# Optimization experiments

Hardware: AMD Instinct MI355X
Metric: run time of the kernel (lower is better)

## Reference

```python
import jax, jax.numpy as jnp
import numpy as np

K = 256
TAU = 1.0


def setup_inputs() -> dict:
    key = jax.random.key(0)
    scores = jax.random.normal(key, (32, 2048), dtype=jnp.float32)
    return {"scores": scores}


def reference(scores) -> jnp.ndarray:
    # scores: [B, dim]
    bsize, dim = scores.shape
    s = scores[:, :, None]  # [B, dim, 1]
    # B_i = sum_j |s_i - s_j|  -> [B, dim, 1]
    A = jnp.abs(s - scores[:, None, :])  # [B, dim, dim]
    Bsum = jnp.sum(A, axis=-1, keepdims=True)  # [B, dim, 1]
    # scaling: (dim + 1 - 2*(i+1)) for i in 0..k-1
    scaling = (dim + 1 - 2 * (jnp.arange(K) + 1)).astype(scores.dtype)  # [k]
    C = s * scaling[None, None, :]  # [B, dim, k] (outer product)
    P_max = jnp.transpose(C - Bsum, (0, 2, 1))  # [B, k, dim]
    P_hat = jax.nn.softmax(P_max / TAU, axis=-1)
    return P_hat
```

## Files before the change

### kernel.cpp

```cpp
#include <hip/hip_runtime.h>
#include <math.h>

#define DIM 2048
#define NB 32
#define NK 256

typedef float vf4 __attribute__((ext_vector_type(4)));

__global__ __launch_bounds__(256) void bsum_kernel(const float* __restrict__ scores,
                                                   float* __restrict__ bsum) {
    __shared__ vf4 srow[128];
    const int b  = blockIdx.z;
    const int j0 = blockIdx.y * 512;
    const int i0 = blockIdx.x * 1024;
    const float* __restrict__ row = scores + b * DIM;

    if (threadIdx.x < 128) srow[threadIdx.x] = ((const vf4*)(row + j0))[threadIdx.x];
    __syncthreads();

    const vf4 xi = ((const vf4*)(row + i0))[threadIdx.x];
    float a0 = 0.f, a1 = 0.f, a2 = 0.f, a3 = 0.f;
    #pragma unroll 4
    for (int jj = 0; jj < 128; ++jj) {
        const vf4 xj = srow[jj];
        a0 += (fabsf(xi.x - xj.x) + fabsf(xi.x - xj.y)) + (fabsf(xi.x - xj.z) + fabsf(xi.x - xj.w));
        a1 += (fabsf(xi.y - xj.x) + fabsf(xi.y - xj.y)) + (fabsf(xi.y - xj.z) + fabsf(xi.y - xj.w));
        a2 += (fabsf(xi.z - xj.x) + fabsf(xi.z - xj.y)) + (fabsf(xi.z - xj.z) + fabsf(xi.z - xj.w));
        a3 += (fabsf(xi.w - xj.x) + fabsf(xi.w - xj.y)) + (fabsf(xi.w - xj.z) + fabsf(xi.w - xj.w));
    }
    float* dst = bsum + b * DIM + i0 + threadIdx.x * 4;
    atomicAdd(dst + 0, a0);
    atomicAdd(dst + 1, a1);
    atomicAdd(dst + 2, a2);
    atomicAdd(dst + 3, a3);
}

__global__ __launch_bounds__(256) void softmax_kernel(const float* __restrict__ scores,
                                                      const float* __restrict__ bsum,
                                                      float* __restrict__ out) {
    const int b = blockIdx.y;
    const int w = threadIdx.x >> 6;
    const int t = threadIdx.x & 63;
    const int k = blockIdx.x * 4 + w;
    const float scale = (float)(DIM - 1 - 2 * k);

    const vf4* __restrict__ s4  = (const vf4*)(scores + b * DIM);
    const vf4* __restrict__ bs4 = (const vf4*)(bsum   + b * DIM);

    float e[32];
    #pragma unroll
    for (int q = 0; q < 8; ++q) {
        const vf4 sv = s4[t + 64 * q];
        const vf4 bv = bs4[t + 64 * q];
        e[4 * q + 0] = fmaf(sv.x, scale, -bv.x);
        e[4 * q + 1] = fmaf(sv.y, scale, -bv.y);
        e[4 * q + 2] = fmaf(sv.z, scale, -bv.z);
        e[4 * q + 3] = fmaf(sv.w, scale, -bv.w);
    }

    float m0 = e[0], m1 = e[1], m2 = e[2], m3 = e[3];
    #pragma unroll
    for (int j = 4; j < 32; j += 4) {
        m0 = fmaxf(m0, e[j + 0]);
        m1 = fmaxf(m1, e[j + 1]);
        m2 = fmaxf(m2, e[j + 2]);
        m3 = fmaxf(m3, e[j + 3]);
    }
    float m = fmaxf(fmaxf(m0, m1), fmaxf(m2, m3));
    #pragma unroll
    for (int off = 32; off > 0; off >>= 1) m = fmaxf(m, __shfl_xor(m, off, 64));

    float s0 = 0.f, s1 = 0.f, s2 = 0.f, s3 = 0.f;
    #pragma unroll
    for (int j = 0; j < 32; j += 4) {
        e[j + 0] = __expf(e[j + 0] - m); s0 += e[j + 0];
        e[j + 1] = __expf(e[j + 1] - m); s1 += e[j + 1];
        e[j + 2] = __expf(e[j + 2] - m); s2 += e[j + 2];
        e[j + 3] = __expf(e[j + 3] - m); s3 += e[j + 3];
    }
    float s = (s0 + s1) + (s2 + s3);
    #pragma unroll
    for (int off = 32; off > 0; off >>= 1) s += __shfl_xor(s, off, 64);

    const float inv = 1.f / s;
    vf4* o4 = (vf4*)(out + ((size_t)(b * NK + k)) * DIM);
    #pragma unroll
    for (int q = 0; q < 8; ++q) {
        vf4 o;
        o.x = e[4 * q + 0] * inv;
        o.y = e[4 * q + 1] * inv;
        o.z = e[4 * q + 2] * inv;
        o.w = e[4 * q + 3] * inv;
        o4[t + 64 * q] = o;
    }
}

extern "C" void kernel_launch(void* const* d_in, const int* in_sizes, int n_in,
                              void* d_out, int out_size, void* d_ws, size_t ws_size,
                              hipStream_t stream) {
    const float* scores = (const float*)d_in[0];
    float* out  = (float*)d_out;
    float* bsum = (float*)d_ws;

    hipMemsetAsync(bsum, 0, (size_t)NB * DIM * sizeof(float), stream);
    bsum_kernel<<<dim3(2, 4, NB), 256, 0, stream>>>(scores, bsum);
    softmax_kernel<<<dim3(NK / 4, NB), 256, 0, stream>>>(scores, bsum, out);
}
```

Measured before the change: 92.52 us.

## Compute Bsum with one thread per element over the full row, drop atomics and memset

The bsum kernel now assigns one thread per output element and has it loop over the whole row, reading scores through wavefront-uniform global vector loads instead of a shared-memory tile. This removes the split-j partial sums, the atomicAdd reduction, and the preceding hipMemsetAsync, so one launch disappears. In exchange there are 512 blocks of 128 threads and each thread handles one i rather than four, so loads are amortised less and each thread runs a 512-iteration serial loop.

```diff
diff --git a/kernel.cpp b/kernel.cpp
--- a/kernel.cpp
+++ b/kernel.cpp
@@ -7,32 +7,24 @@
 
 typedef float vf4 __attribute__((ext_vector_type(4)));
 
-__global__ __launch_bounds__(256) void bsum_kernel(const float* __restrict__ scores,
+__global__ __launch_bounds__(128) void bsum_kernel(const float* __restrict__ scores,
                                                    float* __restrict__ bsum) {
-    __shared__ vf4 srow[128];
-    const int b  = blockIdx.z;
-    const int j0 = blockIdx.y * 512;
-    const int i0 = blockIdx.x * 1024;
+    const int b = blockIdx.y;
+    const int i = blockIdx.x * 128 + (int)threadIdx.x;
     const float* __restrict__ row = scores + b * DIM;
+    const float xi = row[i];
+    const vf4* __restrict__ r4 = (const vf4*)row;
 
-    if (threadIdx.x < 128) srow[threadIdx.x] = ((const vf4*)(row + j0))[threadIdx.x];
-    __syncthreads();
-
-    const vf4 xi = ((const vf4*)(row + i0))[threadIdx.x];
     float a0 = 0.f, a1 = 0.f, a2 = 0.f, a3 = 0.f;
-    #pragma unroll 4
-    for (int jj = 0; jj < 128; ++jj) {
-        const vf4 xj = srow[jj];
-        a0 += (fabsf(xi.x - xj.x) + fabsf(xi.x - xj.y)) + (fabsf(xi.x - xj.z) + fabsf(xi.x - xj.w));
-        a1 += (fabsf(xi.y - xj.x) + fabsf(xi.y - xj.y)) + (fabsf(xi.y - xj.z) + fabsf(xi.y - xj.w));
-        a2 += (fabsf(xi.z - xj.x) + fabsf(xi.z - xj.y)) + (fabsf(xi.z - xj.z) + fabsf(xi.z - xj.w));
-        a3 += (fabsf(xi.w - xj.x) + fabsf(xi.w - xj.y)) + (fabsf(xi.w - xj.z) + fabsf(xi.w - xj.w));
+    #pragma unroll 8
+    for (int j = 0; j < DIM / 4; ++j) {
+        const vf4 xj = r4[j];
+        a0 += fabsf(xi - xj.x);
+        a1 += fabsf(xi - xj.y);
+        a2 += fabsf(xi - xj.z);
+        a3 += fabsf(xi - xj.w);
     }
-    float* dst = bsum + b * DIM + i0 + threadIdx.x * 4;
-    atomicAdd(dst + 0, a0);
-    atomicAdd(dst + 1, a1);
-    atomicAdd(dst + 2, a2);
-    atomicAdd(dst + 3, a3);
+    bsum[b * DIM + i] = (a0 + a1) + (a2 + a3);
 }
 
 __global__ __launch_bounds__(256) void softmax_kernel(const float* __restrict__ scores,
@@ -102,7 +94,6 @@
     float* out  = (float*)d_out;
     float* bsum = (float*)d_ws;
 
-    hipMemsetAsync(bsum, 0, (size_t)NB * DIM * sizeof(float), stream);
-    bsum_kernel<<<dim3(2, 4, NB), 256, 0, stream>>>(scores, bsum);
+    bsum_kernel<<<dim3(16, NB), 128, 0, stream>>>(scores, bsum);
     softmax_kernel<<<dim3(NK / 4, NB), 256, 0, stream>>>(scores, bsum, out);
 }
```

Result: slower. 107.3 us (+15.9%).
